# Performance work log

Measured on AMD Instinct MI355X. Metric: run time of the kernel, lower is better.

Reference implementation:

```python
import jax, jax.numpy as jnp
import numpy as np

EPSILON = 0.1
MAX_ITERATIONS = 100


def setup_inputs() -> dict:
    key = jax.random.key(0)
    k1, k2 = jax.random.split(key)
    x = jax.random.normal(k1, (16, 3, 2048), dtype=jnp.float32)
    y = jax.random.normal(k2, (16, 3, 2048), dtype=jnp.float32)
    return {"x": x, "y": y}


def reference(x, y):
    # x, y: (B, D, N) channels-first point clouds -> (B, N, D)
    xt = jnp.swapaxes(x, 1, 2)
    yt = jnp.swapaxes(y, 1, 2)
    B, N, _ = xt.shape
    # squared euclidean cost: (B, N, N)
    x2 = jnp.sum(xt * xt, axis=-1)  # (B, N)
    y2 = jnp.sum(yt * yt, axis=-1)  # (B, N)
    C = x2[:, :, None] + y2[:, None, :] - 2.0 * jnp.einsum('bnd,bmd->bnm', xt, yt)
    C = jnp.maximum(C, 0.0)  # cdist clamps negatives from cancellation
    K = jnp.exp(-C / EPSILON)

    inv_n = 1.0 / N
    u0 = jnp.full((B, N), inv_n, dtype=x.dtype)
    v0 = jnp.full((B, N), inv_n, dtype=x.dtype)

    def step(carry, _):
        u, _v = carry
        v = inv_n / (jnp.einsum('bnm,bn->bm', K, u) + 1e-8)  # K^T u
        u = inv_n / (jnp.einsum('bnm,bm->bn', K, v) + 1e-8)  # K v
        return (u, v), None

    (u, v), _ = jax.lax.scan(step, (u0, v0), None, length=MAX_ITERATIONS)
    # sum(plan * C) / B where plan = u[:,:,None] * K * v[:,None,:]
    return jnp.einsum('bn,bnm,bm->', u, K * C, v) / B
```

## Files before the change

kernel.cpp:

```cpp
#include <hip/hip_runtime.h>

#define NB 16
#define NN 2048
#define G  64
#define ITERS 100

typedef float v2f __attribute__((ext_vector_type(2)));

static constexpr float INV_N = 1.0f / (float)NN;
static constexpr float NEG_INV_EPS = -10.0f;

__device__ __forceinline__ float fastrcp(float x) { return __builtin_amdgcn_rcpf(x); }

__device__ __forceinline__ void dec4(unsigned int u, float& f0, float& f1, float& f2, float& f3) {
    v2f lo = __builtin_amdgcn_cvt_pk_f32_fp8((int)u, false);
    v2f hi = __builtin_amdgcn_cvt_pk_f32_fp8((int)u, true);
    f0 = lo[0]; f1 = lo[1]; f2 = hi[0]; f3 = hi[1];
}

__global__ __launch_bounds__(256) void build_K(const float* __restrict__ x,
                                               const float* __restrict__ y,
                                               unsigned char* __restrict__ K8,
                                               float* __restrict__ INVS) {
    const int n = blockIdx.x, b = blockIdx.y, tid = threadIdx.x;
    const int w = tid >> 6, l = tid & 63;
    const float* xb = x + (size_t)b * 3 * NN;
    const float* yb = y + (size_t)b * 3 * NN;
    const float x0 = xb[n], x1 = xb[NN + n], x2 = xb[2 * NN + n];
    const float xs = x0 * x0 + x1 * x1 + x2 * x2;
    const int m0 = tid * 8;

    const float4 a0 = *(const float4*)(yb + m0);
    const float4 a1 = *(const float4*)(yb + m0 + 4);
    const float4 b0 = *(const float4*)(yb + NN + m0);
    const float4 b1 = *(const float4*)(yb + NN + m0 + 4);
    const float4 c0 = *(const float4*)(yb + 2 * NN + m0);
    const float4 c1 = *(const float4*)(yb + 2 * NN + m0 + 4);
    const float yy0[8] = {a0.x, a0.y, a0.z, a0.w, a1.x, a1.y, a1.z, a1.w};
    const float yy1[8] = {b0.x, b0.y, b0.z, b0.w, b1.x, b1.y, b1.z, b1.w};
    const float yy2[8] = {c0.x, c0.y, c0.z, c0.w, c1.x, c1.y, c1.z, c1.w};

    float k[8];
#pragma unroll
    for (int j = 0; j < 8; ++j) {
        const float ys  = yy0[j] * yy0[j] + yy1[j] * yy1[j] + yy2[j] * yy2[j];
        const float dot = x0 * yy0[j] + x1 * yy1[j] + x2 * yy2[j];
        const float C   = fmaxf(xs + ys - 2.0f * dot, 0.0f);
        k[j] = __expf(NEG_INV_EPS * C);
    }

    float mx = fmaxf(fmaxf(fmaxf(k[0], k[1]), fmaxf(k[2], k[3])),
                     fmaxf(fmaxf(k[4], k[5]), fmaxf(k[6], k[7])));
#pragma unroll
    for (int off = 32; off > 0; off >>= 1) mx = fmaxf(mx, __shfl_xor(mx, off, 64));
    __shared__ float red[4];
    if (l == 0) red[w] = mx;
    __syncthreads();
    mx = fmaxf(fmaxf(red[0], red[1]), fmaxf(red[2], red[3]));
    mx = fmaxf(mx, 1e-30f);
    const int e = (int)((__float_as_uint(mx) >> 23) & 0xffu) - 127;
    const float sc = __uint_as_float((unsigned)(127 - e) << 23);
    if (tid == 0) INVS[b * NN + n] = __uint_as_float((unsigned)(127 + e) << 23);

    int p0 = __builtin_amdgcn_cvt_pk_fp8_f32(k[0] * sc, k[1] * sc, 0, false);
    p0     = __builtin_amdgcn_cvt_pk_fp8_f32(k[2] * sc, k[3] * sc, p0, true);
    int p1 = __builtin_amdgcn_cvt_pk_fp8_f32(k[4] * sc, k[5] * sc, 0, false);
    p1     = __builtin_amdgcn_cvt_pk_fp8_f32(k[6] * sc, k[7] * sc, p1, true);
    uint2 pk; pk.x = (unsigned)p0; pk.y = (unsigned)p1;
    *(uint2*)(K8 + ((size_t)(b * NN + n)) * NN + m0) = pk;
}

__global__ __launch_bounds__(256) void reduce_v(const float* __restrict__ PART,
                                                float* __restrict__ VV) {
    const int t = blockIdx.x * 256 + threadIdx.x;
    const int b = t >> 11, m = t & (NN - 1);
    const float* p = PART + (size_t)(b * G) * NN + m;
    float s = 0.0f;
#pragma unroll 8
    for (int g = 0; g < G; ++g) s += p[(size_t)g * NN];
    VV[t] = INV_N * fastrcp(s + 1e-8f);
}

__global__ __launch_bounds__(256) void fused_pass(const unsigned char* __restrict__ K8,
                                                  const float* __restrict__ VV,
                                                  const float* __restrict__ INVS,
                                                  float* __restrict__ u_out,
                                                  float* __restrict__ PART,
                                                  int first) {
    const int g = blockIdx.x, b = blockIdx.y, tid = threadIdx.x;
    const int w = tid >> 6, l = tid & 63;

    float v[4][8];
    if (!first) {
        const float* vb = VV + b * NN;
#pragma unroll
        for (int s = 0; s < 4; ++s) {
            const float4 p0 = *(const float4*)(vb + s * 512 + l * 8);
            const float4 p1 = *(const float4*)(vb + s * 512 + l * 8 + 4);
            v[s][0] = p0.x; v[s][1] = p0.y; v[s][2] = p0.z; v[s][3] = p0.w;
            v[s][4] = p1.x; v[s][5] = p1.y; v[s][6] = p1.z; v[s][7] = p1.w;
        }
    }

    float acc[4][8];
#pragma unroll
    for (int s = 0; s < 4; ++s)
#pragma unroll
        for (int j = 0; j < 8; ++j) acc[s][j] = 0.0f;

    const int row0 = g * 32 + w * 8;
    const unsigned char* Kb = K8 + ((size_t)(b * NN + row0)) * NN + l * 8;
    const float* invp = INVS + b * NN + row0;

#pragma unroll 2
    for (int r = 0; r < 8; ++r) {
        uint2 kv[4];
#pragma unroll
        for (int s = 0; s < 4; ++s) kv[s] = *(const uint2*)(Kb + (size_t)r * NN + s * 512);
        const float invs = invp[r];

        float u;
        if (first) {
            u = INV_N;
        } else {
            float d0 = 0, d1 = 0, d2 = 0, d3 = 0, d4 = 0, d5 = 0, d6 = 0, d7 = 0;
#pragma unroll
            for (int s = 0; s < 4; ++s) {
                float f0, f1, f2, f3, f4, f5, f6, f7;
                dec4(kv[s].x, f0, f1, f2, f3);
                dec4(kv[s].y, f4, f5, f6, f7);
                d0 = fmaf(f0, v[s][0], d0); d1 = fmaf(f1, v[s][1], d1);
                d2 = fmaf(f2, v[s][2], d2); d3 = fmaf(f3, v[s][3], d3);
                d4 = fmaf(f4, v[s][4], d4); d5 = fmaf(f5, v[s][5], d5);
                d6 = fmaf(f6, v[s][6], d6); d7 = fmaf(f7, v[s][7], d7);
            }
            float d = ((d0 + d1) + (d2 + d3)) + ((d4 + d5) + (d6 + d7));
#pragma unroll
            for (int off = 32; off > 0; off >>= 1) d += __shfl_xor(d, off, 64);
            u = INV_N * fastrcp(d * invs + 1e-8f);
        }
        const float uw = u * invs;
        if (l == 0) u_out[b * NN + row0 + r] = uw;

#pragma unroll
        for (int s = 0; s < 4; ++s) {
            float f0, f1, f2, f3, f4, f5, f6, f7;
            dec4(kv[s].x, f0, f1, f2, f3);
            dec4(kv[s].y, f4, f5, f6, f7);
            acc[s][0] = fmaf(f0, uw, acc[s][0]); acc[s][1] = fmaf(f1, uw, acc[s][1]);
            acc[s][2] = fmaf(f2, uw, acc[s][2]); acc[s][3] = fmaf(f3, uw, acc[s][3]);
            acc[s][4] = fmaf(f4, uw, acc[s][4]); acc[s][5] = fmaf(f5, uw, acc[s][5]);
            acc[s][6] = fmaf(f6, uw, acc[s][6]); acc[s][7] = fmaf(f7, uw, acc[s][7]);
        }
    }

    __shared__ float lds[4][NN];
#pragma unroll
    for (int s = 0; s < 4; ++s) {
        *(float4*)&lds[w][s * 512 + l * 8]     = make_float4(acc[s][0], acc[s][1], acc[s][2], acc[s][3]);
        *(float4*)&lds[w][s * 512 + l * 8 + 4] = make_float4(acc[s][4], acc[s][5], acc[s][6], acc[s][7]);
    }
    __syncthreads();
    float o[8];
#pragma unroll
    for (int j = 0; j < 8; ++j)
        o[j] = (lds[0][tid * 8 + j] + lds[1][tid * 8 + j]) +
               (lds[2][tid * 8 + j] + lds[3][tid * 8 + j]);
    float* p = PART + ((size_t)(b * G + g)) * NN + tid * 8;
    *(float4*)(p)     = make_float4(o[0], o[1], o[2], o[3]);
    *(float4*)(p + 4) = make_float4(o[4], o[5], o[6], o[7]);
}

__global__ __launch_bounds__(256) void final_sum(const unsigned char* __restrict__ K8,
                                                 const float* __restrict__ x,
                                                 const float* __restrict__ y,
                                                 const float* __restrict__ VV,
                                                 const float* __restrict__ u_in,
                                                 float* __restrict__ out) {
    const int g = blockIdx.x, b = blockIdx.y, tid = threadIdx.x;
    const int w = tid >> 6, l = tid & 63;
    const float* vb = VV + b * NN;

    float v[4][8];
#pragma unroll
    for (int s = 0; s < 4; ++s) {
        const float4 p0 = *(const float4*)(vb + s * 512 + l * 8);
        const float4 p1 = *(const float4*)(vb + s * 512 + l * 8 + 4);
        v[s][0] = p0.x; v[s][1] = p0.y; v[s][2] = p0.z; v[s][3] = p0.w;
        v[s][4] = p1.x; v[s][5] = p1.y; v[s][6] = p1.z; v[s][7] = p1.w;
    }

    const float* xb = x + (size_t)b * 3 * NN;
    const float* yb = y + (size_t)b * 3 * NN;
    float lacc = 0.0f;

    for (int r = 0; r < 8; ++r) {
        const int n = g * 32 + w * 8 + r;
        const float x0 = xb[n], x1 = xb[NN + n], x2 = xb[2 * NN + n];
        const float xs = x0 * x0 + x1 * x1 + x2 * x2;
        const float uwn = u_in[b * NN + n];
        const unsigned char* Kp = K8 + ((size_t)(b * NN + n)) * NN + l * 8;
        float racc = 0.0f;
#pragma unroll
        for (int s = 0; s < 4; ++s) {
            const int m0 = s * 512 + l * 8;
            const uint2 kv = *(const uint2*)(Kp + s * 512);
            float ky[8];
            dec4(kv.x, ky[0], ky[1], ky[2], ky[3]);
            dec4(kv.y, ky[4], ky[5], ky[6], ky[7]);
            const float4 a0 = *(const float4*)(yb + m0);
            const float4 a1 = *(const float4*)(yb + m0 + 4);
            const float4 b0 = *(const float4*)(yb + NN + m0);
            const float4 b1 = *(const float4*)(yb + NN + m0 + 4);
            const float4 c0 = *(const float4*)(yb + 2 * NN + m0);
            const float4 c1 = *(const float4*)(yb + 2 * NN + m0 + 4);
            const float yy0[8] = {a0.x, a0.y, a0.z, a0.w, a1.x, a1.y, a1.z, a1.w};
            const float yy1[8] = {b0.x, b0.y, b0.z, b0.w, b1.x, b1.y, b1.z, b1.w};
            const float yy2[8] = {c0.x, c0.y, c0.z, c0.w, c1.x, c1.y, c1.z, c1.w};
#pragma unroll
            for (int j = 0; j < 8; ++j) {
                const float ys  = yy0[j] * yy0[j] + yy1[j] * yy1[j] + yy2[j] * yy2[j];
                const float dot = x0 * yy0[j] + x1 * yy1[j] + x2 * yy2[j];
                const float C   = fmaxf(xs + ys - 2.0f * dot, 0.0f);
                racc = fmaf(ky[j] * C, v[s][j], racc);
            }
        }
        lacc = fmaf(uwn, racc, lacc);
    }
#pragma unroll
    for (int off = 32; off > 0; off >>= 1) lacc += __shfl_xor(lacc, off, 64);
    __shared__ float red[4];
    if (l == 0) red[w] = lacc;
    __syncthreads();
    if (tid == 0) atomicAdd(out, (red[0] + red[1] + red[2] + red[3]) * (1.0f / (float)NB));
}

extern "C" void kernel_launch(void* const* d_in, const int* in_sizes, int n_in,
                              void* d_out, int out_size, void* d_ws, size_t ws_size,
                              hipStream_t stream) {
    const float* x = (const float*)d_in[0];
    const float* y = (const float*)d_in[1];
    float* out = (float*)d_out;
    char* ws = (char*)d_ws;

    unsigned char* K8 = (unsigned char*)ws;
    const size_t KBYTES = (size_t)NB * NN * NN;
    float* PART = (float*)(ws + KBYTES);
    const size_t PARTN = (size_t)NB * G * NN;
    float* VV   = PART + PARTN;
    float* ub   = VV + (size_t)NB * NN;
    float* INVS = ub + (size_t)NB * NN;

    hipMemsetAsync(out, 0, sizeof(float), stream);

    build_K<<<dim3(NN, NB), 256, 0, stream>>>(x, y, K8, INVS);

    fused_pass<<<dim3(G, NB), 256, 0, stream>>>(K8, VV, INVS, ub, PART, 1);
    for (int i = 0; i < ITERS; ++i) {
        reduce_v<<<dim3(NB * NN / 256), 256, 0, stream>>>(PART, VV);
        fused_pass<<<dim3(G, NB), 256, 0, stream>>>(K8, VV, INVS, ub, PART, 0);
    }
    final_sum<<<dim3(G, NB), 256, 0, stream>>>(K8, x, y, VV, ub, out);
}
```

Measured before the change: 2.477 ms.

## Widen K loads to 16 bytes, process row pairs, vectorize reduce_v

```diff
diff --git a/kernel.cpp b/kernel.cpp
--- a/kernel.cpp
+++ b/kernel.cpp
@@ -73,13 +73,52 @@
 __global__ __launch_bounds__(256) void reduce_v(const float* __restrict__ PART,
                                                 float* __restrict__ VV) {
     const int t = blockIdx.x * 256 + threadIdx.x;
-    const int b = t >> 11, m = t & (NN - 1);
-    const float* p = PART + (size_t)(b * G) * NN + m;
-    float s = 0.0f;
+    const int b = t >> 9;
+    const int m4 = (t & 511) << 2;
+    const float* p = PART + (size_t)(b * G) * NN + m4;
+    float s0 = 0, s1 = 0, s2 = 0, s3 = 0;
 #pragma unroll 8
-    for (int g = 0; g < G; ++g) s += p[(size_t)g * NN];
-    VV[t] = INV_N * fastrcp(s + 1e-8f);
-}
+    for (int g = 0; g < G; ++g) {
+        const float4 q = *(const float4*)(p + (size_t)g * NN);
+        s0 += q.x; s1 += q.y; s2 += q.z; s3 += q.w;
+    }
+    float4 o;
+    o.x = INV_N * fastrcp(s0 + 1e-8f);
+    o.y = INV_N * fastrcp(s1 + 1e-8f);
+    o.z = INV_N * fastrcp(s2 + 1e-8f);
+    o.w = INV_N * fastrcp(s3 + 1e-8f);
+    *(float4*)(VV + (size_t)b * NN + m4) = o;
+}
+
+#define DOT16(kk, vv) {                                                        \
+    float f0_, f1_, f2_, f3_;                                                  \
+    dec4(kk.x, f0_, f1_, f2_, f3_);                                            \
+    d0 = fmaf(f0_, vv[0], d0);  d1 = fmaf(f1_, vv[1], d1);                     \
+    d2 = fmaf(f2_, vv[2], d2);  d3 = fmaf(f3_, vv[3], d3);                     \
+    dec4(kk.y, f0_, f1_, f2_, f3_);                                            \
+    d0 = fmaf(f0_, vv[4], d0);  d1 = fmaf(f1_, vv[5], d1);                     \
+    d2 = fmaf(f2_, vv[6], d2);  d3 = fmaf(f3_, vv[7], d3);                     \
+    dec4(kk.z, f0_, f1_, f2_, f3_);                                            \
+    d0 = fmaf(f0_, vv[8], d0);  d1 = fmaf(f1_, vv[9], d1);                     \
+    d2 = fmaf(f2_, vv[10], d2); d3 = fmaf(f3_, vv[11], d3);                    \
+    dec4(kk.w, f0_, f1_, f2_, f3_);                                            \
+    d0 = fmaf(f0_, vv[12], d0); d1 = fmaf(f1_, vv[13], d1);                    \
+    d2 = fmaf(f2_, vv[14], d2); d3 = fmaf(f3_, vv[15], d3); }
+
+#define ACC16(kk, aa, uu) {                                                    \
+    float f0_, f1_, f2_, f3_;                                                  \
+    dec4(kk.x, f0_, f1_, f2_, f3_);                                            \
+    aa[0] = fmaf(f0_, uu, aa[0]);   aa[1] = fmaf(f1_, uu, aa[1]);              \
+    aa[2] = fmaf(f2_, uu, aa[2]);   aa[3] = fmaf(f3_, uu, aa[3]);              \
+    dec4(kk.y, f0_, f1_, f2_, f3_);                                            \
+    aa[4] = fmaf(f0_, uu, aa[4]);   aa[5] = fmaf(f1_, uu, aa[5]);              \
+    aa[6] = fmaf(f2_, uu, aa[6]);   aa[7] = fmaf(f3_, uu, aa[7]);              \
+    dec4(kk.z, f0_, f1_, f2_, f3_);                                            \
+    aa[8] = fmaf(f0_, uu, aa[8]);   aa[9] = fmaf(f1_, uu, aa[9]);              \
+    aa[10] = fmaf(f2_, uu, aa[10]); aa[11] = fmaf(f3_, uu, aa[11]);            \
+    dec4(kk.w, f0_, f1_, f2_, f3_);                                            \
+    aa[12] = fmaf(f0_, uu, aa[12]); aa[13] = fmaf(f1_, uu, aa[13]);            \
+    aa[14] = fmaf(f2_, uu, aa[14]); aa[15] = fmaf(f3_, uu, aa[15]); }
 
 __global__ __launch_bounds__(256) void fused_pass(const unsigned char* __restrict__ K8,
                                                   const float* __restrict__ VV,
@@ -90,75 +129,79 @@
     const int g = blockIdx.x, b = blockIdx.y, tid = threadIdx.x;
     const int w = tid >> 6, l = tid & 63;
 
-    float v[4][8];
+    float v[2][16];
     if (!first) {
-        const float* vb = VV + b * NN;
-#pragma unroll
-        for (int s = 0; s < 4; ++s) {
-            const float4 p0 = *(const float4*)(vb + s * 512 + l * 8);
-            const float4 p1 = *(const float4*)(vb + s * 512 + l * 8 + 4);
-            v[s][0] = p0.x; v[s][1] = p0.y; v[s][2] = p0.z; v[s][3] = p0.w;
-            v[s][4] = p1.x; v[s][5] = p1.y; v[s][6] = p1.z; v[s][7] = p1.w;
+        const float* vb = VV + b * NN + l * 16;
+#pragma unroll
+        for (int h = 0; h < 2; ++h) {
+            const float4 q0 = *(const float4*)(vb + h * 1024);
+            const float4 q1 = *(const float4*)(vb + h * 1024 + 4);
+            const float4 q2 = *(const float4*)(vb + h * 1024 + 8);
+            const float4 q3 = *(const float4*)(vb + h * 1024 + 12);
+            v[h][0]  = q0.x; v[h][1]  = q0.y; v[h][2]  = q0.z; v[h][3]  = q0.w;
+            v[h][4]  = q1.x; v[h][5]  = q1.y; v[h][6]  = q1.z; v[h][7]  = q1.w;
+            v[h][8]  = q2.x; v[h][9]  = q2.y; v[h][10] = q2.z; v[h][11] = q2.w;
+            v[h][12] = q3.x; v[h][13] = q3.y; v[h][14] = q3.z; v[h][15] = q3.w;
         }
     }
 
-    float acc[4][8];
-#pragma unroll
-    for (int s = 0; s < 4; ++s)
-#pragma unroll
-        for (int j = 0; j < 8; ++j) acc[s][j] = 0.0f;
+    float acc0[16], acc1[16];
+#pragma unroll
+    for (int j = 0; j < 16; ++j) { acc0[j] = 0.0f; acc1[j] = 0.0f; }
 
     const int row0 = g * 32 + w * 8;
-    const unsigned char* Kb = K8 + ((size_t)(b * NN + row0)) * NN + l * 8;
+    const unsigned char* Kb = K8 + ((size_t)(b * NN + row0)) * NN + l * 16;
     const float* invp = INVS + b * NN + row0;
 
-#pragma unroll 2
-    for (int r = 0; r < 8; ++r) {
-        uint2 kv[4];
-#pragma unroll
-        for (int s = 0; s < 4; ++s) kv[s] = *(const uint2*)(Kb + (size_t)r * NN + s * 512);
-        const float invs = invp[r];
-
-        float u;
+#pragma unroll
+    for (int rp = 0; rp < 4; ++rp) {
+        const unsigned char* pA = Kb + (size_t)(2 * rp) * NN;
+        const unsigned char* pB = pA + NN;
+        const uint4 kA0 = *(const uint4*)(pA);
+        const uint4 kA1 = *(const uint4*)(pA + 1024);
+        const uint4 kB0 = *(const uint4*)(pB);
+        const uint4 kB1 = *(const uint4*)(pB + 1024);
+        const float invsA = invp[2 * rp];
+        const float invsB = invp[2 * rp + 1];
+
+        float uwA, uwB;
         if (first) {
-            u = INV_N;
+            uwA = INV_N * invsA;
+            uwB = INV_N * invsB;
         } else {
-            float d0 = 0, d1 = 0, d2 = 0, d3 = 0, d4 = 0, d5 = 0, d6 = 0, d7 = 0;
-#pragma unroll
-            for (int s = 0; s < 4; ++s) {
-                float f0, f1, f2, f3, f4, f5, f6, f7;
-                dec4(kv[s].x, f0, f1, f2, f3);
-                dec4(kv[s].y, f4, f5, f6, f7);
-                d0 = fmaf(f0, v[s][0], d0); d1 = fmaf(f1, v[s][1], d1);
-                d2 = fmaf(f2, v[s][2], d2); d3 = fmaf(f3, v[s][3], d3);
-                d4 = fmaf(f4, v[s][4], d4); d5 = fmaf(f5, v[s][5], d5);
-                d6 = fmaf(f6, v[s][6], d6); d7 = fmaf(f7, v[s][7], d7);
+            float d0 = 0, d1 = 0, d2 = 0, d3 = 0;
+            DOT16(kA0, v[0]); DOT16(kA1, v[1]);
+            float dA = (d0 + d1) + (d2 + d3);
+            d0 = 0; d1 = 0; d2 = 0; d3 = 0;
+            DOT16(kB0, v[0]); DOT16(kB1, v[1]);
+            float dB = (d0 + d1) + (d2 + d3);
+#pragma unroll
+            for (int off = 32; off > 0; off >>= 1) {
+                dA += __shfl_xor(dA, off, 64);
+                dB += __shfl_xor(dB, off, 64);
             }
-            float d = ((d0 + d1) + (d2 + d3)) + ((d4 + d5) + (d6 + d7));
-#pragma unroll
-            for (int off = 32; off > 0; off >>= 1) d += __shfl_xor(d, off, 64);
-            u = INV_N * fastrcp(d * invs + 1e-8f);
+            uwA = INV_N * fastrcp(dA * invsA + 1e-8f) * invsA;
+            uwB = INV_N * fastrcp(dB * invsB + 1e-8f) * invsB;
         }
-        const float uw = u * invs;
-        if (l == 0) u_out[b * NN + row0 + r] = uw;
-
-#pragma unroll
-        for (int s = 0; s < 4; ++s) {
-            float f0, f1, f2, f3, f4, f5, f6, f7;
-            dec4(kv[s].x, f0, f1, f2, f3);
-            dec4(kv[s].y, f4, f5, f6, f7);
-            acc[s][0] = fmaf(f0, uw, acc[s][0]); acc[s][1] = fmaf(f1, uw, acc[s][1]);
-            acc[s][2] = fmaf(f2, uw, acc[s][2]); acc[s][3] = fmaf(f3, uw, acc[s][3]);
-            acc[s][4] = fmaf(f4, uw, acc[s][4]); acc[s][5] = fmaf(f5, uw, acc[s][5]);
-            acc[s][6] = fmaf(f6, uw, acc[s][6]); acc[s][7] = fmaf(f7, uw, acc[s][7]);
+        if (l == 0) {
+            u_out[b * NN + row0 + 2 * rp]     = uwA;
+            u_out[b * NN + row0 + 2 * rp + 1] = uwB;
         }
+        ACC16(kA0, acc0, uwA); ACC16(kA1, acc1, uwA);
+        ACC16(kB0, acc0, uwB); ACC16(kB1, acc1, uwB);
     }
 
     __shared__ float lds[4][NN];
-#pragma unroll
-    for (int s = 0; s < 4; ++s) {
-        *(float4*)&lds[w][s * 512 + l * 8]     = make_float4(acc[s][0], acc[s][1], acc[s][2], acc[s][3]);
-        *(float4*)&lds[w][s * 512 + l * 8 + 4] = make_float4(acc[s][4], acc[s][5], acc[s][6], acc[s][7]);
+    {
+        float* dst = &lds[w][l * 16];
+        *(float4*)(dst)          = make_float4(acc0[0],  acc0[1],  acc0[2],  acc0[3]);
+        *(float4*)(dst + 4)      = make_float4(acc0[4],  acc0[5],  acc0[6],  acc0[7]);
+        *(float4*)(dst + 8)      = make_float4(acc0[8],  acc0[9],  acc0[10], acc0[11]);
+        *(float4*)(dst + 12)     = make_float4(acc0[12], acc0[13], acc0[14], acc0[15]);
+        *(float4*)(dst + 1024)      = make_float4(acc1[0],  acc1[1],  acc1[2],  acc1[3]);
+        *(float4*)(dst + 1024 + 4)  = make_float4(acc1[4],  acc1[5],  acc1[6],  acc1[7]);
+        *(float4*)(dst + 1024 + 8)  = make_float4(acc1[8],  acc1[9],  acc1[10], acc1[11]);
+        *(float4*)(dst + 1024 + 12) = make_float4(acc1[12], acc1[13], acc1[14], acc1[15]);
     }
     __syncthreads();
     float o[8];
@@ -257,7 +300,7 @@
 
     fused_pass<<<dim3(G, NB), 256, 0, stream>>>(K8, VV, INVS, ub, PART, 1);
     for (int i = 0; i < ITERS; ++i) {
-        reduce_v<<<dim3(NB * NN / 256), 256, 0, stream>>>(PART, VV);
+        reduce_v<<<dim3(NB * NN / 4 / 256), 256, 0, stream>>>(PART, VV);
         fused_pass<<<dim3(G, NB), 256, 0, stream>>>(K8, VV, INVS, ub, PART, 0);
     }
     final_sum<<<dim3(G, NB), 256, 0, stream>>>(K8, x, y, VV, ub, out);
```

Measured after the change: 3.022 ms. 22.0% more time.
